# Kernel optimization log

Hardware: AMD Instinct MI355X
Metric: run time of the kernel (lower is better)

Reference implementation:

```python
import jax, jax.numpy as jnp
import numpy as np

B, S, H, D = 32, 512, 768, 64  # batch, seq_len, hidden_size, inner_dim
BIG = 1e12


def _rope(x, sin_pos, cos_pos):
    # x: [B,S,D]; rotate pairs: [-x1, x0, -x3, x2, ...]
    x2 = jnp.stack([-x[..., 1::2], x[..., ::2]], axis=-1).reshape(x.shape)
    return x * cos_pos + x2 * sin_pos


def setup_inputs() -> dict:
    key = jax.random.key(0)
    k1, k2, k3 = jax.random.split(key, 3)
    hidden = jax.random.normal(k1, (B, S, H), dtype=jnp.float32)
    attention_mask = jnp.ones((B, S), dtype=jnp.float32)
    span_ids = jax.random.randint(k2, (B, S, S), 0, 2).astype(jnp.int32)
    dense_w = jax.random.normal(k3, (H, 2 * D), dtype=jnp.float32) * 0.02
    dense_b = jnp.zeros((2 * D,), dtype=jnp.float32)
    return {"hidden": hidden, "attention_mask": attention_mask,
            "span_ids": span_ids, "dense_w": dense_w, "dense_b": dense_b}


def reference(hidden, attention_mask, span_ids, dense_w, dense_b):
    b, s, _ = hidden.shape
    out = hidden @ dense_w + dense_b            # [B,S,2D]
    qw, kw = out[..., :D], out[..., D:]
    # sinusoidal position embedding, interleaved [s0,c0,s1,c1,...]
    pos = jnp.arange(s, dtype=jnp.float32)[:, None]              # [S,1]
    inv_freq = 10000.0 ** (-2.0 * jnp.arange(D // 2, dtype=jnp.float32) / D)
    ang = pos * inv_freq                                         # [S,D/2]
    sin_pos = jnp.repeat(jnp.sin(ang), 2, axis=-1)[None]         # [1,S,D]
    cos_pos = jnp.repeat(jnp.cos(ang), 2, axis=-1)[None]
    qw = _rope(qw, sin_pos, cos_pos)
    kw = _rope(kw, sin_pos, cos_pos)
    logits = jnp.einsum('bmd,bnd->bmn', qw, kw)                  # [B,S,S]
    pad = attention_mask[:, None, :]                             # mask keys (n)
    logits = logits * pad - (1.0 - pad) * BIG
    tril = jnp.tril(jnp.ones((s, s), logits.dtype), -1)          # strict lower
    logits = logits - tril * BIG
    logits = logits / (D ** 0.5)
    # multilabel categorical crossentropy over rows [B*S, S]
    y_true = span_ids.astype(logits.dtype).reshape(b * s, -1)
    y_pred = logits.reshape(b * s, -1)
    yp = (1.0 - 2.0 * y_true) * y_pred
    zeros = jnp.zeros((b * s, 1), yp.dtype)
    y_neg = jnp.concatenate([yp - y_true * BIG, zeros], axis=-1)
    y_pos = jnp.concatenate([yp - (1.0 - y_true) * BIG, zeros], axis=-1)
    loss = (jax.nn.logsumexp(y_neg, axis=-1) + jax.nn.logsumexp(y_pos, axis=-1)).mean()
    return loss
```

## Files before the change

kernel.cpp:

```cpp
#include <hip/hip_runtime.h>
#include <hip/hip_bf16.h>
#include <math.h>

#define Bb   32
#define Ss   512
#define Hh   768
#define Dd   64
#define ND   128
#define Mrows (Bb*Ss)
#define BIGF 1.0e12f

typedef __attribute__((ext_vector_type(8))) short short8;
typedef __attribute__((ext_vector_type(4))) float floatx4;

__device__ __forceinline__ short f2bf(float x) {
    unsigned u = __builtin_bit_cast(unsigned, x);
    u = (u + 0x7FFF + ((u >> 16) & 1)) >> 16;
    return (short)u;
}

__global__ __launch_bounds__(256) void prep_kernel(
    const float* __restrict__ w, short* __restrict__ wfrag,
    float2* __restrict__ rt)
{
    int idx = blockIdx.x * 256 + threadIdx.x;
    int j    = idx & 7;
    int lane = (idx >> 3) & 63;
    int rest = idx >> 9;
    int c    = rest % 24;
    int tt   = rest / 24;
    int n    = tt * 16 + (lane & 15);
    int k    = c * 32 + (lane >> 4) * 8 + j;
    wfrag[idx] = f2bf(w[k * ND + n]);
    if (idx < Ss * 32) {
        int spos = idx >> 5;
        int i    = idx & 31;
        float ln_base = -logf(10000.0f) / 32.0f;
        float invf = expf(ln_base * (float)i);
        float sn, cs;
        sincosf((float)spos * invf, &sn, &cs);
        rt[idx] = make_float2(sn, cs);
    }
}

__global__ __launch_bounds__(256) void pack_kernel(
    const int* __restrict__ span, unsigned* __restrict__ spack)
{
    int gid = blockIdx.x * 256 + threadIdx.x;
    int lane = threadIdx.x & 63;
    unsigned long long m = __ballot(span[gid] != 0);
    if ((gid & 31) == 0)
        spack[gid >> 5] = (unsigned)(m >> (lane & 32));
}

__global__ __launch_bounds__(512, 4) void proj_rope_kernel(
    const float*  __restrict__ hidden,
    const short*  __restrict__ wfrag,
    const float*  __restrict__ bias,
    const float2* __restrict__ rt,
    short* __restrict__ qbf,
    short* __restrict__ kbf)
{
    const int tid   = threadIdx.x;
    const int w     = tid >> 6;
    const int lane  = tid & 63;
    const int quad  = lane >> 4;
    const int l15   = lane & 15;
    const int rg    = w & 1;
    const int h     = (w >> 1) & 1;
    const int kh    = w >> 2;
    const int mrow0 = blockIdx.x * 32 + rg * 16;

    const float* ap  = hidden + (size_t)(mrow0 + l15) * Hh + quad * 8
                              + kh * 12 * 32;
    const short* bp0 = wfrag + (size_t)(h * 4) * 24 * 512 + lane * 8
                             + kh * 12 * 512;

    floatx4 acc[4] = {{0.f,0.f,0.f,0.f},{0.f,0.f,0.f,0.f},
                      {0.f,0.f,0.f,0.f},{0.f,0.f,0.f,0.f}};

    float4 A0[2], A1[2];
    short8 Bf[2][4];

#define PLOAD(buf, c) do {                                        \
    A0[buf] = *(const float4*)(ap + (c) * 32);                    \
    A1[buf] = *(const float4*)(ap + (c) * 32 + 4);                \
    Bf[buf][0] = *(const short8*)(bp0 + 0 * 24 * 512 + (c) * 512);\
    Bf[buf][1] = *(const short8*)(bp0 + 1 * 24 * 512 + (c) * 512);\
    Bf[buf][2] = *(const short8*)(bp0 + 2 * 24 * 512 + (c) * 512);\
    Bf[buf][3] = *(const short8*)(bp0 + 3 * 24 * 512 + (c) * 512);\
} while (0)

#define PCOMP(buf) do {                                         \
    short8 av;                                                  \
    av[0] = f2bf(A0[buf].x); av[1] = f2bf(A0[buf].y);           \
    av[2] = f2bf(A0[buf].z); av[3] = f2bf(A0[buf].w);           \
    av[4] = f2bf(A1[buf].x); av[5] = f2bf(A1[buf].y);           \
    av[6] = f2bf(A1[buf].z); av[7] = f2bf(A1[buf].w);           \
    acc[0] = __builtin_amdgcn_mfma_f32_16x16x32_bf16(av, Bf[buf][0], acc[0], 0, 0, 0); \
    acc[1] = __builtin_amdgcn_mfma_f32_16x16x32_bf16(av, Bf[buf][1], acc[1], 0, 0, 0); \
    acc[2] = __builtin_amdgcn_mfma_f32_16x16x32_bf16(av, Bf[buf][2], acc[2], 0, 0, 0); \
    acc[3] = __builtin_amdgcn_mfma_f32_16x16x32_bf16(av, Bf[buf][3], acc[3], 0, 0, 0); \
} while (0)

    PLOAD(0, 0);
    #pragma unroll
    for (int cc = 0; cc < 6; ++cc) {
        if (2 * cc + 1 < 12) PLOAD(1, 2 * cc + 1);
        PCOMP(0);
        if (2 * cc + 2 < 12) PLOAD(0, 2 * cc + 2);
        PCOMP(1);
    }
#undef PLOAD
#undef PCOMP

    __shared__ float lacc[4][16][64];
    const int slot = w & 3;
    if (kh == 1) {
        #pragma unroll
        for (int t = 0; t < 4; ++t)
            #pragma unroll
            for (int reg = 0; reg < 4; ++reg)
                lacc[slot][t * 4 + reg][lane] = acc[t][reg];
    }
    __syncthreads();
    if (kh == 1) return;

    #pragma unroll
    for (int t = 0; t < 4; ++t)
        #pragma unroll
        for (int reg = 0; reg < 4; ++reg)
            acc[t][reg] += lacc[slot][t * 4 + reg][lane];

    short* dst = h ? kbf : qbf;
    const float* bptr = bias + h * 64;

    #pragma unroll
    for (int t = 0; t < 4; ++t) {
        const int d  = t * 16 + l15;
        const float bz = bptr[d];
        const float2* rtp = rt + (d >> 1);
        #pragma unroll
        for (int reg = 0; reg < 4; ++reg) {
            const int grow = mrow0 + quad * 4 + reg;
            const int spos = grow & (Ss - 1);
            float2 sc = rtp[spos * 32];
            float x  = acc[t][reg] + bz;
            float xo = __shfl_xor(x, 1);
            float o  = (d & 1) ? (x * sc.y + xo * sc.x)
                               : (x * sc.y - xo * sc.x);
            dst[(size_t)grow * Dd + d] = f2bf(o);
        }
    }
}

__global__ __launch_bounds__(512, 4) void span_loss_kernel(
    const short* __restrict__ qbf,
    const short* __restrict__ kbf,
    const float* __restrict__ mask,
    const unsigned* __restrict__ spack,
    double* __restrict__ rowsum)
{
    const int b    = blockIdx.x >> 4;
    const int m0   = (blockIdx.x & 15) * 32;
    const int tid  = threadIdx.x;
    const int w    = tid >> 6;
    const int lane = tid & 63;
    const int quad = lane >> 4;
    const int l15  = lane & 15;
    const int rh   = w & 1;
    const int cg   = w >> 1;
    const int rbase = m0 + rh * 16;
    const int cbase = cg * 128;

    __shared__ float part[2][4][32];
    __shared__ float bred[2][32];

    const short* qp = qbf + (size_t)(b * Ss + rbase + l15) * Dd + quad * 8;
    short8 a0 = *(const short8*)(qp);
    short8 a1 = *(const short8*)(qp + 32);

    unsigned spw[4][4];
    float pdv[8];
    {
        const unsigned* spp = spack
            + (size_t)(b * Ss + rbase + quad * 4) * 16 + cg * 4;
        #pragma unroll
        for (int reg = 0; reg < 4; ++reg)
            #pragma unroll
            for (int g = 0; g < 4; ++g)
                spw[reg][g] = spp[reg * 16 + g];
        #pragma unroll
        for (int t = 0; t < 8; ++t)
            pdv[t] = mask[b * Ss + cbase + t * 16 + l15];
    }

    floatx4 acc[8];
    #pragma unroll
    for (int t = 0; t < 8; ++t) acc[t] = (floatx4){0.f, 0.f, 0.f, 0.f};

    const short* kp = kbf + (size_t)(b * Ss + cbase + l15) * Dd + quad * 8;
    #pragma unroll
    for (int t = 0; t < 8; ++t) {
        short8 bv = *(const short8*)(kp + (size_t)t * 16 * Dd);
        acc[t] = __builtin_amdgcn_mfma_f32_16x16x32_bf16(a0, bv, acc[t], 0, 0, 0);
    }
    #pragma unroll
    for (int t = 0; t < 8; ++t) {
        short8 bv = *(const short8*)(kp + (size_t)t * 16 * Dd + 32);
        acc[t] = __builtin_amdgcn_mfma_f32_16x16x32_bf16(a1, bv, acc[t], 0, 0, 0);
    }

    unsigned spb = 0;
    #pragma unroll
    for (int t = 0; t < 8; ++t) {
        const int n = cbase + t * 16 + l15;
        const float pd = pdv[t];
        const int sh = (t & 1) * 16 + l15;
        #pragma unroll
        for (int reg = 0; reg < 4; ++reg) {
            const int m = rbase + quad * 4 + reg;
            unsigned bit = (spw[reg][t >> 1] >> sh) & 1u;
            float logit = acc[t][reg] * pd - (1.0f - pd) * BIGF;
            if (n < m) logit -= BIGF;
            logit *= 0.125f;
            float ft = (float)bit;
            acc[t][reg] = (1.0f - 2.0f * ft) * logit;
            spb |= bit << (t * 4 + reg);
        }
    }

    float mxn[4] = {0.f, 0.f, 0.f, 0.f};
    float mxp[4] = {0.f, 0.f, 0.f, 0.f};
    #pragma unroll
    for (int t = 0; t < 8; ++t) {
        #pragma unroll
        for (int reg = 0; reg < 4; ++reg) {
            float ft = (float)((spb >> (t * 4 + reg)) & 1u);
            float yp = acc[t][reg];
            mxn[reg] = fmaxf(mxn[reg], yp - ft * BIGF);
            mxp[reg] = fmaxf(mxp[reg], yp - (1.0f - ft) * BIGF);
        }
    }
    #pragma unroll
    for (int off = 1; off < 16; off <<= 1) {
        #pragma unroll
        for (int reg = 0; reg < 4; ++reg) {
            mxn[reg] = fmaxf(mxn[reg], __shfl_xor(mxn[reg], off));
            mxp[reg] = fmaxf(mxp[reg], __shfl_xor(mxp[reg], off));
        }
    }
    if (l15 == 0) {
        #pragma unroll
        for (int reg = 0; reg < 4; ++reg) {
            part[0][cg][rh * 16 + quad * 4 + reg] = mxn[reg];
            part[1][cg][rh * 16 + quad * 4 + reg] = mxp[reg];
        }
    }
    __syncthreads();
    if (tid < 64) {
        int np = tid >> 5, r = tid & 31;
        float mv = fmaxf(fmaxf(part[np][0][r], part[np][1][r]),
                         fmaxf(part[np][2][r], part[np][3][r]));
        bred[np][r] = mv;
    }
    __syncthreads();

    float bmn[4], bmp[4];
    #pragma unroll
    for (int reg = 0; reg < 4; ++reg) {
        bmn[reg] = bred[0][rh * 16 + quad * 4 + reg];
        bmp[reg] = bred[1][rh * 16 + quad * 4 + reg];
    }
    float smn[4] = {0.f, 0.f, 0.f, 0.f};
    float smp[4] = {0.f, 0.f, 0.f, 0.f};
    #pragma unroll
    for (int t = 0; t < 8; ++t) {
        #pragma unroll
        for (int reg = 0; reg < 4; ++reg) {
            float ft = (float)((spb >> (t * 4 + reg)) & 1u);
            float yp = acc[t][reg];
            smn[reg] += __expf(yp - ft * BIGF - bmn[reg]);
            smp[reg] += __expf(yp - (1.0f - ft) * BIGF - bmp[reg]);
        }
    }
    #pragma unroll
    for (int off = 1; off < 16; off <<= 1) {
        #pragma unroll
        for (int reg = 0; reg < 4; ++reg) {
            smn[reg] += __shfl_xor(smn[reg], off);
            smp[reg] += __shfl_xor(smp[reg], off);
        }
    }
    if (l15 == 0) {
        #pragma unroll
        for (int reg = 0; reg < 4; ++reg) {
            part[0][cg][rh * 16 + quad * 4 + reg] = smn[reg];
            part[1][cg][rh * 16 + quad * 4 + reg] = smp[reg];
        }
    }
    __syncthreads();

    if (tid < 32) {
        int r = tid;
        float SN = __expf(-bred[0][r])
                 + part[0][0][r] + part[0][1][r] + part[0][2][r] + part[0][3][r];
        float SP = __expf(-bred[1][r])
                 + part[1][0][r] + part[1][1][r] + part[1][2][r] + part[1][3][r];
        float lse = (bred[0][r] + logf(SN)) + (bred[1][r] + logf(SP));
        rowsum[(size_t)(b * Ss + m0 + r)] = (double)lse;
    }
}

__global__ __launch_bounds__(1024) void final_reduce_kernel(
    const double* __restrict__ rowsum, float* __restrict__ out)
{
    __shared__ double sh[1024];
    const int tid = threadIdx.x;
    double s = 0.0;
    #pragma unroll
    for (int i = 0; i < 16; ++i) s += rowsum[tid + i * 1024];
    sh[tid] = s;
    __syncthreads();
    for (int off = 512; off > 0; off >>= 1) {
        if (tid < off) sh[tid] += sh[tid + off];
        __syncthreads();
    }
    if (tid == 0) out[0] = (float)(sh[0] / (double)Mrows);
}

extern "C" void kernel_launch(void* const* d_in, const int* in_sizes, int n_in,
                              void* d_out, int out_size, void* d_ws, size_t ws_size,
                              hipStream_t stream)
{
    const float* hidden = (const float*)d_in[0];
    const float* mask   = (const float*)d_in[1];
    const int*   span   = (const int*)  d_in[2];
    const float* w      = (const float*)d_in[3];
    const float* bias   = (const float*)d_in[4];
    float* out = (float*)d_out;

    char* p = (char*)d_ws;
    double*   rowsum = (double*)p;          p += 131072;
    short*    wfrag  = (short*)p;           p += 196608;
    float2*   rt     = (float2*)p;          p += 131072;
    unsigned* spack  = (unsigned*)p;        p += (size_t)Mrows * 16 * 4;
    short*    qbf    = (short*)p;           p += (size_t)Mrows * Dd * 2;
    short*    kbf    = (short*)p;

    prep_kernel<<<Hh * ND / 256, 256, 0, stream>>>(w, wfrag, rt);
    pack_kernel<<<Mrows * Ss / 256, 256, 0, stream>>>(span, spack);
    proj_rope_kernel<<<Mrows / 32, 512, 0, stream>>>(hidden, wfrag, bias, rt, qbf, kbf);
    span_loss_kernel<<<Bb * 16, 512, 0, stream>>>(qbf, kbf, mask, spack, rowsum);
    final_reduce_kernel<<<1, 1024, 0, stream>>>(rowsum, out);
}
```

Baseline: 152.3 us.

## Read span ids directly in loss kernel, fuse final reduction, prescale q

Removes the separate pack kernel that bit-packed span_ids. The loss kernel now loads the int32 span values directly, which saves one full write and read pass over the packed buffer. The final reduction kernel is replaced by per-block partial sums plus a last-block-done atomic counter, and the counter is reset in prep_kernel. Also folds the 1/sqrt(D) scale into q during projection and simplifies the masking arithmetic with selects. Each loss block now issues more scattered 4-byte span loads, and the last-block pattern depends on fences.

```diff
diff --git a/kernel.cpp b/kernel.cpp
--- a/kernel.cpp
+++ b/kernel.cpp
@@ -8,7 +8,9 @@
 #define Dd   64
 #define ND   128
 #define Mrows (Bb*Ss)
-#define BIGF 1.0e12f
+#define BIGF  1.0e12f
+#define BIG8F 1.25e11f
+#define NEGHUGE -1.0e30f
 
 typedef __attribute__((ext_vector_type(8))) short short8;
 typedef __attribute__((ext_vector_type(4))) float floatx4;
@@ -21,7 +23,8 @@
 
 __global__ __launch_bounds__(256) void prep_kernel(
     const float* __restrict__ w, short* __restrict__ wfrag,
-    float2* __restrict__ rt)
+    float2* __restrict__ rt, double* __restrict__ partial,
+    unsigned* __restrict__ cnt)
 {
     int idx = blockIdx.x * 256 + threadIdx.x;
     int j    = idx & 7;
@@ -41,16 +44,8 @@
         sincosf((float)spos * invf, &sn, &cs);
         rt[idx] = make_float2(sn, cs);
     }
-}
-
-__global__ __launch_bounds__(256) void pack_kernel(
-    const int* __restrict__ span, unsigned* __restrict__ spack)
-{
-    int gid = blockIdx.x * 256 + threadIdx.x;
-    int lane = threadIdx.x & 63;
-    unsigned long long m = __ballot(span[gid] != 0);
-    if ((gid & 31) == 0)
-        spack[gid >> 5] = (unsigned)(m >> (lane & 32));
+    if (idx < 512) partial[idx] = 0.0;
+    if (idx == 512) *cnt = 0u;
 }
 
 __global__ __launch_bounds__(512, 4) void proj_rope_kernel(
@@ -134,6 +129,7 @@
 
     short* dst = h ? kbf : qbf;
     const float* bptr = bias + h * 64;
+    const float qs = h ? 1.0f : 0.125f;
 
     #pragma unroll
     for (int t = 0; t < 4; ++t) {
@@ -149,7 +145,7 @@
             float xo = __shfl_xor(x, 1);
             float o  = (d & 1) ? (x * sc.y + xo * sc.x)
                                : (x * sc.y - xo * sc.x);
-            dst[(size_t)grow * Dd + d] = f2bf(o);
+            dst[(size_t)grow * Dd + d] = f2bf(o * qs);
         }
     }
 }
@@ -158,8 +154,10 @@
     const short* __restrict__ qbf,
     const short* __restrict__ kbf,
     const float* __restrict__ mask,
-    const unsigned* __restrict__ spack,
-    double* __restrict__ rowsum)
+    const int*   __restrict__ span,
+    double* __restrict__ partial,
+    unsigned* __restrict__ cnt,
+    float* __restrict__ out)
 {
     const int b    = blockIdx.x >> 4;
     const int m0   = (blockIdx.x & 15) * 32;
@@ -175,26 +173,26 @@
 
     __shared__ float part[2][4][32];
     __shared__ float bred[2][32];
+    __shared__ int   isLast;
+
+    int spv[8][4];
+    float pdv[8];
+    {
+        const int* spp = span + ((size_t)(b * Ss + rbase + quad * 4)) * Ss
+                              + cbase + l15;
+        #pragma unroll
+        for (int t = 0; t < 8; ++t) {
+            pdv[t] = mask[b * Ss + cbase + t * 16 + l15];
+            #pragma unroll
+            for (int reg = 0; reg < 4; ++reg)
+                spv[t][reg] = spp[(size_t)reg * Ss + t * 16];
+        }
+    }
 
     const short* qp = qbf + (size_t)(b * Ss + rbase + l15) * Dd + quad * 8;
     short8 a0 = *(const short8*)(qp);
     short8 a1 = *(const short8*)(qp + 32);
 
-    unsigned spw[4][4];
-    float pdv[8];
-    {
-        const unsigned* spp = spack
-            + (size_t)(b * Ss + rbase + quad * 4) * 16 + cg * 4;
-        #pragma unroll
-        for (int reg = 0; reg < 4; ++reg)
-            #pragma unroll
-            for (int g = 0; g < 4; ++g)
-                spw[reg][g] = spp[reg * 16 + g];
-        #pragma unroll
-        for (int t = 0; t < 8; ++t)
-            pdv[t] = mask[b * Ss + cbase + t * 16 + l15];
-    }
-
     floatx4 acc[8];
     #pragma unroll
     for (int t = 0; t < 8; ++t) acc[t] = (floatx4){0.f, 0.f, 0.f, 0.f};
@@ -216,17 +214,14 @@
     for (int t = 0; t < 8; ++t) {
         const int n = cbase + t * 16 + l15;
         const float pd = pdv[t];
-        const int sh = (t & 1) * 16 + l15;
         #pragma unroll
         for (int reg = 0; reg < 4; ++reg) {
             const int m = rbase + quad * 4 + reg;
-            unsigned bit = (spw[reg][t >> 1] >> sh) & 1u;
-            float logit = acc[t][reg] * pd - (1.0f - pd) * BIGF;
-            if (n < m) logit -= BIGF;
-            logit *= 0.125f;
-            float ft = (float)bit;
-            acc[t][reg] = (1.0f - 2.0f * ft) * logit;
-            spb |= bit << (t * 4 + reg);
+            const int sv = spv[t][reg];
+            float logit = acc[t][reg] * pd - (1.0f - pd) * BIG8F;
+            if (n < m) logit -= BIG8F;
+            acc[t][reg] = sv ? -logit : logit;
+            spb |= (unsigned)(sv != 0) << (t * 4 + reg);
         }
     }
 
@@ -236,10 +231,10 @@
     for (int t = 0; t < 8; ++t) {
         #pragma unroll
         for (int reg = 0; reg < 4; ++reg) {
-            float ft = (float)((spb >> (t * 4 + reg)) & 1u);
+            bool f = (spb >> (t * 4 + reg)) & 1u;
             float yp = acc[t][reg];
-            mxn[reg] = fmaxf(mxn[reg], yp - ft * BIGF);
-            mxp[reg] = fmaxf(mxp[reg], yp - (1.0f - ft) * BIGF);
+            mxn[reg] = fmaxf(mxn[reg], f ? NEGHUGE : yp);
+            mxp[reg] = fmaxf(mxp[reg], f ? yp : NEGHUGE);
         }
     }
     #pragma unroll
@@ -278,10 +273,10 @@
     for (int t = 0; t < 8; ++t) {
         #pragma unroll
         for (int reg = 0; reg < 4; ++reg) {
-            float ft = (float)((spb >> (t * 4 + reg)) & 1u);
+            bool f = (spb >> (t * 4 + reg)) & 1u;
             float yp = acc[t][reg];
-            smn[reg] += __expf(yp - ft * BIGF - bmn[reg]);
-            smp[reg] += __expf(yp - (1.0f - ft) * BIGF - bmp[reg]);
+            smn[reg] += __expf((f ? NEGHUGE : yp) - bmn[reg]);
+            smp[reg] += __expf((f ? yp : NEGHUGE) - bmp[reg]);
         }
     }
     #pragma unroll
@@ -301,32 +296,37 @@
     }
     __syncthreads();
 
+    float lse = 0.0f;
     if (tid < 32) {
         int r = tid;
         float SN = __expf(-bred[0][r])
                  + part[0][0][r] + part[0][1][r] + part[0][2][r] + part[0][3][r];
         float SP = __expf(-bred[1][r])
                  + part[1][0][r] + part[1][1][r] + part[1][2][r] + part[1][3][r];
-        float lse = (bred[0][r] + logf(SN)) + (bred[1][r] + logf(SP));
-        rowsum[(size_t)(b * Ss + m0 + r)] = (double)lse;
-    }
-}
-
-__global__ __launch_bounds__(1024) void final_reduce_kernel(
-    const double* __restrict__ rowsum, float* __restrict__ out)
-{
-    __shared__ double sh[1024];
-    const int tid = threadIdx.x;
-    double s = 0.0;
-    #pragma unroll
-    for (int i = 0; i < 16; ++i) s += rowsum[tid + i * 1024];
-    sh[tid] = s;
-    __syncthreads();
-    for (int off = 512; off > 0; off >>= 1) {
-        if (tid < off) sh[tid] += sh[tid + off];
-        __syncthreads();
-    }
-    if (tid == 0) out[0] = (float)(sh[0] / (double)Mrows);
+        lse = (bred[0][r] + logf(SN)) + (bred[1][r] + logf(SP));
+    }
+    if (tid < 64) {
+        double dv = (tid < 32) ? (double)lse : 0.0;
+        #pragma unroll
+        for (int off = 1; off < 32; off <<= 1) dv += __shfl_xor(dv, off);
+        if (tid == 0) {
+            partial[blockIdx.x] = dv;
+            __threadfence();
+            unsigned old = atomicAdd(cnt, 1u);
+            isLast = (old == 511u) ? 1 : 0;
+        }
+    }
+    __syncthreads();
+
+    if (isLast && tid < 64) {
+        double s = 0.0;
+        #pragma unroll
+        for (int i = 0; i < 8; ++i)
+            s += atomicAdd(&partial[tid + i * 64], 0.0);
+        #pragma unroll
+        for (int off = 1; off < 64; off <<= 1) s += __shfl_xor(s, off);
+        if (tid == 0) out[0] = (float)(s / (double)Mrows);
+    }
 }
 
 extern "C" void kernel_launch(void* const* d_in, const int* in_sizes, int n_in,
@@ -341,16 +341,14 @@
     float* out = (float*)d_out;
 
     char* p = (char*)d_ws;
-    double*   rowsum = (double*)p;          p += 131072;
-    short*    wfrag  = (short*)p;           p += 196608;
-    float2*   rt     = (float2*)p;          p += 131072;
-    unsigned* spack  = (unsigned*)p;        p += (size_t)Mrows * 16 * 4;
-    short*    qbf    = (short*)p;           p += (size_t)Mrows * Dd * 2;
-    short*    kbf    = (short*)p;
-
-    prep_kernel<<<Hh * ND / 256, 256, 0, stream>>>(w, wfrag, rt);
-    pack_kernel<<<Mrows * Ss / 256, 256, 0, stream>>>(span, spack);
+    double*   partial = (double*)p;
+    unsigned* cnt     = (unsigned*)(p + 4096);
+    short*    wfrag   = (short*)(p + 8192);
+    float2*   rt      = (float2*)(p + 8192 + 196608);
+    short*    qbf     = (short*)(p + 8192 + 196608 + 131072);
+    short*    kbf     = qbf + (size_t)Mrows * Dd;
+
+    prep_kernel<<<Hh * ND / 256, 256, 0, stream>>>(w, wfrag, rt, partial, cnt);
     proj_rope_kernel<<<Mrows / 32, 512, 0, stream>>>(hidden, wfrag, bias, rt, qbf, kbf);
-    span_loss_kernel<<<Bb * 16, 512, 0, stream>>>(qbf, kbf, mask, spack, rowsum);
-    final_reduce_kernel<<<1, 1024, 0, stream>>>(rowsum, out);
-}
+    span_loss_kernel<<<Bb * 16, 512, 0, stream>>>(qbf, kbf, mask, span, partial, cnt, out);
+}
```

Measured after the change: 153.0 us. Within noise of the previous version (+0.5%).
